# Kernel tuning notes

Hardware: AMD Instinct MI355X
Metric: run time of the kernel (lower is better)

Reference implementation:

```python
import jax, jax.numpy as jnp
import numpy as np

DIM = 1024
EPS = 1e-5

def _layernorm(x, w, b):
    mu = jnp.mean(x, axis=-1, keepdims=True)
    var = jnp.var(x, axis=-1, keepdims=True)
    return (x - mu) * jax.lax.rsqrt(var + EPS) * w + b

def setup_inputs() -> dict:
    key = jax.random.key(0)
    ks = jax.random.split(key, 16)
    d = DIM
    s = 1.0 / np.sqrt(d)
    inp = {
        "x": jax.random.normal(ks[0], (4, 2048, d), dtype=jnp.float32),
        "ln1_w": jnp.ones((d,), jnp.float32),
        "ln1_b": jnp.zeros((d,), jnp.float32),
        "Wq": jax.random.normal(ks[1], (d, d), jnp.float32) * s,
        "bq": jnp.zeros((d,), jnp.float32),
        "Wk": jax.random.normal(ks[2], (d, d), jnp.float32) * s,
        "bk": jnp.zeros((d,), jnp.float32),
        "Wv": jax.random.normal(ks[3], (d, d), jnp.float32) * s,
        "bv": jnp.zeros((d,), jnp.float32),
        "Wo": jax.random.normal(ks[4], (d, d), jnp.float32) * s,
        "bo": jnp.zeros((d,), jnp.float32),
        "W1": jax.random.normal(ks[5], (d, 4 * d), jnp.float32) * s,
        "b1": jnp.zeros((4 * d,), jnp.float32),
        "W2": jax.random.normal(ks[6], (4 * d, d), jnp.float32) * (0.5 / np.sqrt(d)),
        "b2": jnp.zeros((d,), jnp.float32),
        "ln2_w": jnp.ones((d,), jnp.float32),
        "ln2_b": jnp.zeros((d,), jnp.float32),
    }
    return inp

def reference(x, ln1_w, ln1_b, Wq, bq, Wk, bk, Wv, bv, Wo, bo, W1, b1, W2, b2, ln2_w, ln2_b):
    d = x.shape[-1]
    scale = 1.0 / jnp.sqrt(jnp.asarray(d, x.dtype))
    h = _layernorm(x, ln1_w, ln1_b)
    q = h @ Wq + bq
    k = h @ Wk + bk
    v = h @ Wv + bv
    # [b, s, s] attention scores (single head, full matrix as in original)
    scores = jnp.einsum("bqd,bkd->bqk", q, k) * scale
    attn = jax.nn.softmax(scores, axis=-1)
    ctx = jnp.einsum("bqk,bkd->bqd", attn, v)
    x = x + (ctx @ Wo + bo)
    h2 = _layernorm(x, ln2_w, ln2_b)
    ffn = jax.nn.relu(h2 @ W1 + b1) @ W2 + b2
    return x + ffn
```

## Files before the change

kernel.cpp:

```cpp
#include <hip/hip_runtime.h>


#define EPS 1e-5f
constexpr int D   = 1024;
constexpr int DFF = 4096;
constexpr int NB  = 4;
constexpr int S   = 2048;
constexpr int M   = NB * S;

typedef __bf16 bf16x8 __attribute__((ext_vector_type(8)));
typedef float  f32x4  __attribute__((ext_vector_type(4)));

__device__ __forceinline__ ushort f2bf(float f) {
  uint u = __builtin_bit_cast(uint, f);
  return (ushort)((u + 0x7fffu + ((u >> 16) & 1u)) >> 16);
}
__device__ __forceinline__ float bf2f(ushort h) {
  return __builtin_bit_cast(float, (uint)h << 16);
}
__device__ __forceinline__ void split(float f, ushort& h, ushort& l) {
  h = f2bf(f);
  l = f2bf(f - bf2f(h));
}

#define GLOAD16(g, l)                                                     \
  __builtin_amdgcn_global_load_lds(                                       \
      (const __attribute__((address_space(1))) void*)(g),                 \
      (__attribute__((address_space(3))) void*)(l), 16, 0, 0)

#define LD8(base, off) \
  __builtin_bit_cast(bf16x8, *reinterpret_cast<const uint4*>((base) + (off)))

__global__ __launch_bounds__(256) void ln_kernel(const float* __restrict__ x,
                                                 const float* __restrict__ w,
                                                 const float* __restrict__ b,
                                                 ushort* __restrict__ oh,
                                                 ushort* __restrict__ ol) {
  const int row = blockIdx.x;
  const int t   = threadIdx.x;
  const float4 v = reinterpret_cast<const float4*>(x + (size_t)row * D)[t];
  float s  = v.x + v.y + v.z + v.w;
  float sq = v.x * v.x + v.y * v.y + v.z * v.z + v.w * v.w;
#pragma unroll
  for (int off = 32; off > 0; off >>= 1) {
    s  += __shfl_down(s, off);
    sq += __shfl_down(sq, off);
  }
  __shared__ float red[8];
  if ((t & 63) == 0) { red[t >> 6] = s; red[(t >> 6) + 4] = sq; }
  __syncthreads();
  if (t == 0) {
    float ts = red[0] + red[1] + red[2] + red[3];
    float tq = red[4] + red[5] + red[6] + red[7];
    float mu  = ts * (1.0f / D);
    float var = tq * (1.0f / D) - mu * mu;
    red[0] = mu;
    red[1] = rsqrtf(var + EPS);
  }
  __syncthreads();
  const float mu = red[0], rs = red[1];
  const float4 wv = reinterpret_cast<const float4*>(w)[t];
  const float4 bv = reinterpret_cast<const float4*>(b)[t];
  float o0 = (v.x - mu) * rs * wv.x + bv.x;
  float o1 = (v.y - mu) * rs * wv.y + bv.y;
  float o2 = (v.z - mu) * rs * wv.z + bv.z;
  float o3 = (v.w - mu) * rs * wv.w + bv.w;
  ushort4 hh, ll;
  split(o0, hh.x, ll.x); split(o1, hh.y, ll.y);
  split(o2, hh.z, ll.z); split(o3, hh.w, ll.w);
  *reinterpret_cast<ushort4*>(oh + (size_t)row * D + t * 4) = hh;
  *reinterpret_cast<ushort4*>(ol + (size_t)row * D + t * 4) = ll;
}

__global__ __launch_bounds__(256) void softmax_kernel(const float* __restrict__ sc,
                                                      ushort* __restrict__ oh,
                                                      ushort* __restrict__ ol) {
  const size_t row = blockIdx.x;
  const float* p = sc + row * (size_t)S;
  const int t = threadIdx.x;
  constexpr float scale = 0.03125f;
  float4 a = reinterpret_cast<const float4*>(p)[t];
  float4 b = reinterpret_cast<const float4*>(p)[t + 256];
  a.x *= scale; a.y *= scale; a.z *= scale; a.w *= scale;
  b.x *= scale; b.y *= scale; b.z *= scale; b.w *= scale;
  float m = fmaxf(fmaxf(fmaxf(a.x, a.y), fmaxf(a.z, a.w)),
                  fmaxf(fmaxf(b.x, b.y), fmaxf(b.z, b.w)));
#pragma unroll
  for (int off = 32; off > 0; off >>= 1) m = fmaxf(m, __shfl_xor(m, off));
  __shared__ float redm[4];
  __shared__ float reds[4];
  if ((t & 63) == 0) redm[t >> 6] = m;
  __syncthreads();
  m = fmaxf(fmaxf(redm[0], redm[1]), fmaxf(redm[2], redm[3]));
  a.x = __expf(a.x - m); a.y = __expf(a.y - m);
  a.z = __expf(a.z - m); a.w = __expf(a.w - m);
  b.x = __expf(b.x - m); b.y = __expf(b.y - m);
  b.z = __expf(b.z - m); b.w = __expf(b.w - m);
  float s = a.x + a.y + a.z + a.w + b.x + b.y + b.z + b.w;
#pragma unroll
  for (int off = 32; off > 0; off >>= 1) s += __shfl_xor(s, off);
  if ((t & 63) == 0) reds[t >> 6] = s;
  __syncthreads();
  s = reds[0] + reds[1] + reds[2] + reds[3];
  const float inv = 1.0f / s;
  ushort4 ha, la, hb, lb;
  split(a.x * inv, ha.x, la.x); split(a.y * inv, ha.y, la.y);
  split(a.z * inv, ha.z, la.z); split(a.w * inv, ha.w, la.w);
  split(b.x * inv, hb.x, lb.x); split(b.y * inv, hb.y, lb.y);
  split(b.z * inv, hb.z, lb.z); split(b.w * inv, hb.w, lb.w);
  ushort* ph = oh + row * (size_t)S;
  ushort* pl = ol + row * (size_t)S;
  *reinterpret_cast<ushort4*>(ph + t * 4)        = ha;
  *reinterpret_cast<ushort4*>(ph + 1024 + t * 4) = hb;
  *reinterpret_cast<ushort4*>(pl + t * 4)        = la;
  *reinterpret_cast<ushort4*>(pl + 1024 + t * 4) = lb;
}

__global__ __launch_bounds__(256) void transpose_conv(const float* __restrict__ in,
                                                      ushort* __restrict__ oh,
                                                      ushort* __restrict__ ol,
                                                      int R, int C,
                                                      long long sIn, long long sOut) {
  __shared__ float tile[32][33];
  const int bz = blockIdx.z;
  const float* ip = in + (size_t)bz * sIn;
  ushort* ph = oh + (size_t)bz * sOut;
  ushort* pl = ol + (size_t)bz * sOut;
  const int c0 = blockIdx.x * 32, r0 = blockIdx.y * 32;
  const int tx = threadIdx.x & 31, ty = threadIdx.x >> 5;
#pragma unroll
  for (int i = 0; i < 4; ++i)
    tile[ty + 8 * i][tx] = ip[(size_t)(r0 + ty + 8 * i) * C + c0 + tx];
  __syncthreads();
#pragma unroll
  for (int i = 0; i < 4; ++i) {
    float v = tile[tx][ty + 8 * i];
    ushort h, l;
    split(v, h, l);
    const size_t o = (size_t)(c0 + ty + 8 * i) * R + r0 + tx;
    ph[o] = h;
    pl[o] = l;
  }
}

__global__ __launch_bounds__(256) void transpose_bf(const ushort* __restrict__ ih,
                                                    const ushort* __restrict__ il,
                                                    ushort* __restrict__ oh,
                                                    ushort* __restrict__ ol,
                                                    int R, int C,
                                                    long long sIn, long long sOut) {
  __shared__ ushort th[32][34];
  __shared__ ushort tl[32][34];
  const int bz = blockIdx.z;
  const ushort* ph = ih + (size_t)bz * sIn;
  const ushort* pl = il + (size_t)bz * sIn;
  ushort* qh = oh + (size_t)bz * sOut;
  ushort* ql = ol + (size_t)bz * sOut;
  const int c0 = blockIdx.x * 32, r0 = blockIdx.y * 32;
  const int tx = threadIdx.x & 31, ty = threadIdx.x >> 5;
#pragma unroll
  for (int i = 0; i < 4; ++i) {
    const size_t src = (size_t)(r0 + ty + 8 * i) * C + c0 + tx;
    th[ty + 8 * i][tx] = ph[src];
    tl[ty + 8 * i][tx] = pl[src];
  }
  __syncthreads();
#pragma unroll
  for (int i = 0; i < 4; ++i) {
    const size_t o = (size_t)(c0 + ty + 8 * i) * R + r0 + tx;
    qh[o] = th[tx][ty + 8 * i];
    ql[o] = tl[tx][ty + 8 * i];
  }
}

template <bool HAS_BIAS, bool RELU, bool WRITE_F32, int NSEG>
__global__ __launch_bounds__(512, 2) void gemm256(
    const ushort* __restrict__ Ah, const ushort* __restrict__ Al,
    const ushort* __restrict__ Bth, const ushort* __restrict__ Btl,
    const float* __restrict__ b0, const float* __restrict__ b1,
    const float* __restrict__ b2, float* __restrict__ Cf,
    ushort* __restrict__ Ch0, ushort* __restrict__ Cl0,
    ushort* __restrict__ Ch1, ushort* __restrict__ Cl1,
    ushort* __restrict__ Ch2, ushort* __restrict__ Cl2,
    int N, int K, int ostride, long long sA, long long sB, long long sC) {
  __shared__ __align__(16) ushort sAb[2][256 * 64];
  __shared__ __align__(16) ushort sBb[2][256 * 64];

  const int bz = blockIdx.z;
  const size_t aof = (size_t)bz * sA, bof = (size_t)bz * sB, cof = (size_t)bz * sC;

  const int gx = gridDim.x;
  const int nwg = gx * gridDim.y;
  int lin = blockIdx.y * gx + blockIdx.x;
  lin = (lin & 7) * (nwg >> 3) + (lin >> 3);
  const int bm = (lin / gx) * 256;
  const int bn = (lin % gx) * 256;

  const int tid = threadIdx.x;
  const int lane = tid & 63, w = tid >> 6;
  const int wr = (w >> 2) * 128, wc = (w & 3) * 64;
  const int fr = lane & 15, fc = lane >> 4;

  const int srow  = tid >> 3;
  const int slot  = (tid & 7) ^ (srow & 7);
  const int hilo  = slot >> 2;
  const int kg    = slot & 3;
  const ushort* gA = (hilo ? Al : Ah) + aof + (size_t)(bm + srow) * K + kg * 8;
  const ushort* gB = (hilo ? Btl : Bth) + bof + (size_t)(bn + srow) * K + kg * 8;
  const size_t rstep = (size_t)64 * K;
  const int dsto = tid * 16;

  int aoff[8][2], boff[4][2];
#pragma unroll
  for (int i = 0; i < 8; ++i) {
    const int row = wr + i * 16 + fr;
#pragma unroll
    for (int h = 0; h < 2; ++h)
      aoff[i][h] = row * 128 + (((h * 4 + fc) ^ (row & 7)) * 16);
  }
#pragma unroll
  for (int j = 0; j < 4; ++j) {
    const int row = wc + j * 16 + fr;
#pragma unroll
    for (int h = 0; h < 2; ++h)
      boff[j][h] = row * 128 + (((h * 4 + fc) ^ (row & 7)) * 16);
  }

  f32x4 acc[8][4];
  const f32x4 zero = {0.f, 0.f, 0.f, 0.f};
#pragma unroll
  for (int i = 0; i < 8; ++i)
#pragma unroll
    for (int j = 0; j < 4; ++j) acc[i][j] = zero;

  const int nt = K >> 5;

  {
    char* dA = (char*)(&sAb[0][0]) + dsto;
    char* dB = (char*)(&sBb[0][0]) + dsto;
#pragma unroll
    for (int rr = 0; rr < 4; ++rr) {
      GLOAD16(gA + rr * rstep, dA + rr * 8192);
      GLOAD16(gB + rr * rstep, dB + rr * 8192);
    }
  }

#define MFMA6(ii, xh, xl, jj)                                                 \
  acc[ii][jj] = __builtin_amdgcn_mfma_f32_16x16x32_bf16(xh, bh##jj, acc[ii][jj], 0, 0, 0); \
  acc[ii][jj] = __builtin_amdgcn_mfma_f32_16x16x32_bf16(xh, bl##jj, acc[ii][jj], 0, 0, 0); \
  acc[ii][jj] = __builtin_amdgcn_mfma_f32_16x16x32_bf16(xl, bh##jj, acc[ii][jj], 0, 0, 0);

#define MFMA_PAIR(i0, i1, xh, xl, yh, yl)                                     \
  MFMA6(i0, xh, xl, 0) MFMA6(i1, yh, yl, 0)                                   \
  MFMA6(i0, xh, xl, 1) MFMA6(i1, yh, yl, 1)                                   \
  MFMA6(i0, xh, xl, 2) MFMA6(i1, yh, yl, 2)                                   \
  MFMA6(i0, xh, xl, 3) MFMA6(i1, yh, yl, 3)

  for (int t = 0; t < nt; ++t) {
    const int p = t & 1, q = p ^ 1;
    const bool pf = (t + 1 < nt);
    const int kkn = (t + 1) << 5;
    const ushort* gAn = gA + kkn;
    const ushort* gBn = gB + kkn;
    char* dAq = (char*)(&sAb[q][0]) + dsto;
    char* dBq = (char*)(&sBb[q][0]) + dsto;
    const char* lA = (const char*)(&sAb[p][0]);
    const char* lB = (const char*)(&sBb[p][0]);

    if (pf) {
      GLOAD16(gAn + 0 * rstep, dAq + 0 * 8192);
      GLOAD16(gAn + 1 * rstep, dAq + 1 * 8192);
      asm volatile("s_waitcnt vmcnt(2)" ::: "memory");
    } else {
      asm volatile("s_waitcnt vmcnt(0)" ::: "memory");
    }
    __builtin_amdgcn_s_barrier();

    bf16x8 bh0 = LD8(lB, boff[0][0]), bl0 = LD8(lB, boff[0][1]);
    bf16x8 bh1 = LD8(lB, boff[1][0]), bl1 = LD8(lB, boff[1][1]);
    bf16x8 bh2 = LD8(lB, boff[2][0]), bl2 = LD8(lB, boff[2][1]);
    bf16x8 bh3 = LD8(lB, boff[3][0]), bl3 = LD8(lB, boff[3][1]);
    bf16x8 a0h = LD8(lA, aoff[0][0]), a0l = LD8(lA, aoff[0][1]);
    bf16x8 a1h = LD8(lA, aoff[1][0]), a1l = LD8(lA, aoff[1][1]);
    __builtin_amdgcn_s_barrier();
    __builtin_amdgcn_s_setprio(1);
    MFMA_PAIR(0, 1, a0h, a0l, a1h, a1l)
    __builtin_amdgcn_s_setprio(0);
    __builtin_amdgcn_s_barrier();

    {
      bf16x8 a2h = LD8(lA, aoff[2][0]), a2l = LD8(lA, aoff[2][1]);
      bf16x8 a3h = LD8(lA, aoff[3][0]), a3l = LD8(lA, aoff[3][1]);
      if (pf) {
        GLOAD16(gAn + 2 * rstep, dAq + 2 * 8192);
        GLOAD16(gAn + 3 * rstep, dAq + 3 * 8192);
      }
      __builtin_amdgcn_s_barrier();
      __builtin_amdgcn_s_setprio(1);
      MFMA_PAIR(2, 3, a2h, a2l, a3h, a3l)
      __builtin_amdgcn_s_setprio(0);
      __builtin_amdgcn_s_barrier();
    }
    {
      bf16x8 a4h = LD8(lA, aoff[4][0]), a4l = LD8(lA, aoff[4][1]);
      bf16x8 a5h = LD8(lA, aoff[5][0]), a5l = LD8(lA, aoff[5][1]);
      if (pf) {
        GLOAD16(gBn + 0 * rstep, dBq + 0 * 8192);
        GLOAD16(gBn + 1 * rstep, dBq + 1 * 8192);
      }
      __builtin_amdgcn_s_barrier();
      __builtin_amdgcn_s_setprio(1);
      MFMA_PAIR(4, 5, a4h, a4l, a5h, a5l)
      __builtin_amdgcn_s_setprio(0);
      __builtin_amdgcn_s_barrier();
    }
    {
      bf16x8 a6h = LD8(lA, aoff[6][0]), a6l = LD8(lA, aoff[6][1]);
      bf16x8 a7h = LD8(lA, aoff[7][0]), a7l = LD8(lA, aoff[7][1]);
      if (pf) {
        GLOAD16(gBn + 2 * rstep, dBq + 2 * 8192);
        GLOAD16(gBn + 3 * rstep, dBq + 3 * 8192);
      }
      __builtin_amdgcn_s_barrier();
      __builtin_amdgcn_s_setprio(1);
      MFMA_PAIR(6, 7, a6h, a6l, a7h, a7l)
      __builtin_amdgcn_s_setprio(0);
      __builtin_amdgcn_s_barrier();
    }
  }

#pragma unroll
  for (int j = 0; j < 4; ++j) {
    const int col = bn + wc + j * 16 + fr;
    int lc = col;
    const float* bp = b0;
    ushort* ph = Ch0;
    ushort* pl = Cl0;
    if (NSEG == 3) {
      const int seg = col >> 10;
      lc = col & 1023;
      bp = (seg == 0) ? b0 : (seg == 1 ? b1 : b2);
      ph = (seg == 0) ? Ch0 : (seg == 1 ? Ch1 : Ch2);
      pl = (seg == 0) ? Cl0 : (seg == 1 ? Cl1 : Cl2);
    }
    const float bi = HAS_BIAS ? bp[lc] : 0.0f;
#pragma unroll
    for (int i = 0; i < 8; ++i) {
#pragma unroll
      for (int r = 0; r < 4; ++r) {
        const int row = bm + wr + i * 16 + fc * 4 + r;
        float o = acc[i][j][r] + bi;
        if (RELU) o = fmaxf(o, 0.0f);
        if (WRITE_F32) {
          Cf[cof + (size_t)row * N + col] = o;
        } else {
          ushort hh, ll;
          split(o, hh, ll);
          const size_t idx = (size_t)row * ostride + lc;
          ph[idx] = hh;
          pl[idx] = ll;
        }
      }
    }
  }
#undef MFMA6
#undef MFMA_PAIR
}

template <bool HAS_BIAS, bool RELU, bool HAS_RES, bool WRITE_F32, bool EMIT_BF16>
__global__ __launch_bounds__(256, 2) void gemm_bf16x3(
    const ushort* __restrict__ Ah, const ushort* __restrict__ Al,
    const ushort* __restrict__ Bth, const ushort* __restrict__ Btl,
    const float* __restrict__ bias, const float* Res,
    float* Cf, ushort* __restrict__ Ch, ushort* __restrict__ Cl,
    int N, int K, long long sA, long long sB, long long sC) {
  __shared__ __align__(16) ushort sAh[128 * 32];
  __shared__ __align__(16) ushort sAl[128 * 32];
  __shared__ __align__(16) ushort sBh[128 * 32];
  __shared__ __align__(16) ushort sBl[128 * 32];

  const int bz = blockIdx.z;
  const size_t aof = (size_t)bz * sA, bof = (size_t)bz * sB, cof = (size_t)bz * sC;

  const int gx = gridDim.x;
  const int nwg = gx * gridDim.y;
  int lin = blockIdx.y * gx + blockIdx.x;
  lin = (lin & 7) * (nwg >> 3) + (lin >> 3);
  const int bm = (lin / gx) * 128;
  const int bn = (lin % gx) * 128;

  const int tid = threadIdx.x, w = tid >> 6, lane = tid & 63;
  const int wr = (w >> 1) * 64, wc = (w & 1) * 64;

  const int c0 = w * 2, c1 = c0 + 1;
  const int r0 = c0 * 16 + (lane >> 2);
  const int r1 = r0 + 16;
  const int kc = ((lane & 3) ^ (r0 & 3)) * 8;
  const size_t gA0 = aof + (size_t)(bm + r0) * K + kc;
  const size_t gA1 = aof + (size_t)(bm + r1) * K + kc;
  const size_t gB0 = bof + (size_t)(bn + r0) * K + kc;
  const size_t gB1 = bof + (size_t)(bn + r1) * K + kc;
  ushort* dA0 = sAh + c0 * 512; ushort* dA1 = sAh + c1 * 512;
  ushort* dA2 = sAl + c0 * 512; ushort* dA3 = sAl + c1 * 512;
  ushort* dB0 = sBh + c0 * 512; ushort* dB1 = sBh + c1 * 512;
  ushort* dB2 = sBl + c0 * 512; ushort* dB3 = sBl + c1 * 512;

  const int fr = lane & 15, fc = lane >> 4;
  int aoffB[4], boffB[4];
#pragma unroll
  for (int i = 0; i < 4; ++i) {
    const int ra = wr + i * 16 + fr;
    aoffB[i] = ra * 64 + ((fc ^ (ra & 3)) * 16);
    const int rb = wc + i * 16 + fr;
    boffB[i] = rb * 64 + ((fc ^ (rb & 3)) * 16);
  }

  f32x4 acc[4][4];
  const f32x4 zero = {0.f, 0.f, 0.f, 0.f};
#pragma unroll
  for (int i = 0; i < 4; ++i)
#pragma unroll
    for (int j = 0; j < 4; ++j) acc[i][j] = zero;

  for (int kk = 0; kk < K; kk += 32) {
    GLOAD16(Ah + gA0 + kk, dA0);
    GLOAD16(Ah + gA1 + kk, dA1);
    GLOAD16(Al + gA0 + kk, dA2);
    GLOAD16(Al + gA1 + kk, dA3);
    GLOAD16(Bth + gB0 + kk, dB0);
    GLOAD16(Bth + gB1 + kk, dB1);
    GLOAD16(Btl + gB0 + kk, dB2);
    GLOAD16(Btl + gB1 + kk, dB3);
    __syncthreads();

    bf16x8 fah[4], fal[4], fbh[4], fbl[4];
#pragma unroll
    for (int i = 0; i < 4; ++i) {
      fah[i] = LD8((const char*)sAh, aoffB[i]);
      fal[i] = LD8((const char*)sAl, aoffB[i]);
      fbh[i] = LD8((const char*)sBh, boffB[i]);
      fbl[i] = LD8((const char*)sBl, boffB[i]);
    }
    __syncthreads();

#pragma unroll
    for (int i = 0; i < 4; ++i)
#pragma unroll
      for (int j = 0; j < 4; ++j) {
        acc[i][j] = __builtin_amdgcn_mfma_f32_16x16x32_bf16(fah[i], fbh[j], acc[i][j], 0, 0, 0);
        acc[i][j] = __builtin_amdgcn_mfma_f32_16x16x32_bf16(fah[i], fbl[j], acc[i][j], 0, 0, 0);
        acc[i][j] = __builtin_amdgcn_mfma_f32_16x16x32_bf16(fal[i], fbh[j], acc[i][j], 0, 0, 0);
      }
  }

#pragma unroll
  for (int j = 0; j < 4; ++j) {
    const int col = bn + wc + j * 16 + fr;
    const float bi = HAS_BIAS ? bias[col] : 0.0f;
#pragma unroll
    for (int i = 0; i < 4; ++i) {
#pragma unroll
      for (int r = 0; r < 4; ++r) {
        const int row = bm + wr + i * 16 + fc * 4 + r;
        float o = acc[i][j][r] + bi;
        if (RELU) o = fmaxf(o, 0.0f);
        const size_t idx = cof + (size_t)row * N + col;
        if (HAS_RES) o += Res[idx];
        if (WRITE_F32) Cf[idx] = o;
        if (EMIT_BF16) {
          ushort h, l;
          split(o, h, l);
          Ch[idx] = h;
          Cl[idx] = l;
        }
      }
    }
  }
}

extern "C" void kernel_launch(void* const* d_in, const int* in_sizes, int n_in,
                              void* d_out, int out_size, void* d_ws, size_t ws_size,
                              hipStream_t stream) {
  const float* x     = (const float*)d_in[0];
  const float* ln1_w = (const float*)d_in[1];
  const float* ln1_b = (const float*)d_in[2];
  const float* Wq    = (const float*)d_in[3];
  const float* bq    = (const float*)d_in[4];
  const float* Wk    = (const float*)d_in[5];
  const float* bk    = (const float*)d_in[6];
  const float* Wv    = (const float*)d_in[7];
  const float* bv    = (const float*)d_in[8];
  const float* Wo    = (const float*)d_in[9];
  const float* bo    = (const float*)d_in[10];
  const float* W1    = (const float*)d_in[11];
  const float* b1    = (const float*)d_in[12];
  const float* W2    = (const float*)d_in[13];
  const float* b2    = (const float*)d_in[14];
  const float* ln2_w = (const float*)d_in[15];
  const float* ln2_b = (const float*)d_in[16];
  float* out = (float*)d_out;
  char* W = (char*)d_ws;

  auto U = [&](size_t mb) { return (ushort*)(W + (mb << 20)); };
  auto F = [&](size_t mb) { return (float*)(W + (mb << 20)); };
  ushort *h1h = U(0),   *h1l = U(16);
  ushort *wqkvh = U(32), *wqkvl = U(38);
  ushort *qh  = U(64),  *ql  = U(80);
  ushort *kh  = U(96),  *kl  = U(112);
  ushort *vh  = U(128), *vl  = U(144);
  ushort *vth = U(160), *vtl = U(176);
  float  *scf = F(0);
  ushort *ath = U(64),  *atl = U(96);
  ushort *cxh = U(128), *cxl = U(144);
  ushort *woh = U(0),   *wol = U(2);
  ushort *h2h = U(4),   *h2l = U(20);
  ushort *w1h = U(36),  *w1l = U(44);
  ushort *w2h = U(0),   *w2l = U(8);
  ushort *t1h = U(64),  *t1l = U(128);

  const long long SD = (long long)S * D, SS = (long long)S * S;
  dim3 tb(256);

  transpose_conv<<<dim3(32, 32, 1), tb, 0, stream>>>(Wq, wqkvh, wqkvl, D, D, 0, 0);
  transpose_conv<<<dim3(32, 32, 1), tb, 0, stream>>>(Wk, wqkvh + (size_t)D * D,
                                                     wqkvl + (size_t)D * D, D, D, 0, 0);
  transpose_conv<<<dim3(32, 32, 1), tb, 0, stream>>>(Wv, wqkvh + 2 * (size_t)D * D,
                                                     wqkvl + 2 * (size_t)D * D, D, D, 0, 0);

  ln_kernel<<<M, tb, 0, stream>>>(x, ln1_w, ln1_b, h1h, h1l);

  gemm256<true, false, false, 3><<<dim3(12, 32, 1), 512, 0, stream>>>(
      h1h, h1l, wqkvh, wqkvl, bq, bk, bv, nullptr,
      qh, ql, kh, kl, vh, vl, 3072, D, D, 0, 0, 0);

  transpose_bf<<<dim3(32, 64, NB), tb, 0, stream>>>(vh, vl, vth, vtl, S, D, SD, SD);

  gemm256<false, false, true, 1><<<dim3(8, 8, NB), 512, 0, stream>>>(
      qh, ql, kh, kl, nullptr, nullptr, nullptr, scf,
      nullptr, nullptr, nullptr, nullptr, nullptr, nullptr,
      S, D, S, SD, SD, SS);

  softmax_kernel<<<M, tb, 0, stream>>>(scf, ath, atl);

  gemm_bf16x3<false, false, false, false, true><<<dim3(8, 16, NB), tb, 0, stream>>>(
      ath, atl, vth, vtl, nullptr, nullptr, nullptr, cxh, cxl, D, S, SS, SD, SD);

  transpose_conv<<<dim3(32, 32, 1), tb, 0, stream>>>(Wo, woh, wol, D, D, 0, 0);
  gemm_bf16x3<true, false, true, true, false><<<dim3(8, 64, 1), tb, 0, stream>>>(
      cxh, cxl, woh, wol, bo, x, out, nullptr, nullptr, D, D, 0, 0, 0);

  ln_kernel<<<M, tb, 0, stream>>>(out, ln2_w, ln2_b, h2h, h2l);

  transpose_conv<<<dim3(128, 32, 1), tb, 0, stream>>>(W1, w1h, w1l, D, DFF, 0, 0);

  gemm256<true, true, false, 1><<<dim3(16, 32, 1), 512, 0, stream>>>(
      h2h, h2l, w1h, w1l, b1, nullptr, nullptr, nullptr,
      t1h, t1l, nullptr, nullptr, nullptr, nullptr, DFF, D, DFF, 0, 0, 0);

  transpose_conv<<<dim3(32, 128, 1), tb, 0, stream>>>(W2, w2h, w2l, DFF, D, 0, 0);

  gemm_bf16x3<true, false, true, true, false><<<dim3(8, 64, 1), tb, 0, stream>>>(
      t1h, t1l, w2h, w2l, b2, out, out, nullptr, nullptr, D, DFF, 0, 0, 0);
}
```

Measured before the change: 1.075 ms.

## Double-buffer 128-tile GEMM, simplify gemm256 prefetch, split fused QKV projection

The 128x128 GEMM becomes gemm128p. It holds hi/lo tiles interleaved in a double-buffered, XOR-swizzled LDS layout, prefetches the next K-tile with async global-to-LDS loads, and removes the two __syncthreads per iteration. gemm256 now issues all eight prefetch loads at the top of each iteration and drops several barriers. The fused 3-segment QKV GEMM is replaced by three separate gemm128p launches. The aim is to overlap global loads with MFMA work and cut barrier overhead, but it costs more kernel launches, lower tile reuse for QKV, and possible LDS-reuse hazards from the removed barriers.

Measured after the change: 1.062 ms. No clear change (-1.1%).

```diff
diff --git a/kernel.cpp b/kernel.cpp
--- a/kernel.cpp
+++ b/kernel.cpp
@@ -30,6 +30,17 @@
 
 #define LD8(base, off) \
   __builtin_bit_cast(bf16x8, *reinterpret_cast<const uint4*>((base) + (off)))
+
+#define MFMA6(ii, xh, xl, jj)                                                 \
+  acc[ii][jj] = __builtin_amdgcn_mfma_f32_16x16x32_bf16(xh, bh##jj, acc[ii][jj], 0, 0, 0); \
+  acc[ii][jj] = __builtin_amdgcn_mfma_f32_16x16x32_bf16(xh, bl##jj, acc[ii][jj], 0, 0, 0); \
+  acc[ii][jj] = __builtin_amdgcn_mfma_f32_16x16x32_bf16(xl, bh##jj, acc[ii][jj], 0, 0, 0);
+
+#define MFMA_PAIR(i0, i1, xh, xl, yh, yl)                                     \
+  MFMA6(i0, xh, xl, 0) MFMA6(i1, yh, yl, 0)                                   \
+  MFMA6(i0, xh, xl, 1) MFMA6(i1, yh, yl, 1)                                   \
+  MFMA6(i0, xh, xl, 2) MFMA6(i1, yh, yl, 2)                                   \
+  MFMA6(i0, xh, xl, 3) MFMA6(i1, yh, yl, 3)
 
 __global__ __launch_bounds__(256) void ln_kernel(const float* __restrict__ x,
                                                  const float* __restrict__ w,
@@ -173,15 +184,12 @@
   }
 }
 
-template <bool HAS_BIAS, bool RELU, bool WRITE_F32, int NSEG>
+template <bool HAS_BIAS, bool RELU, bool WRITE_F32>
 __global__ __launch_bounds__(512, 2) void gemm256(
     const ushort* __restrict__ Ah, const ushort* __restrict__ Al,
     const ushort* __restrict__ Bth, const ushort* __restrict__ Btl,
-    const float* __restrict__ b0, const float* __restrict__ b1,
-    const float* __restrict__ b2, float* __restrict__ Cf,
-    ushort* __restrict__ Ch0, ushort* __restrict__ Cl0,
-    ushort* __restrict__ Ch1, ushort* __restrict__ Cl1,
-    ushort* __restrict__ Ch2, ushort* __restrict__ Cl2,
+    const float* __restrict__ bias, float* __restrict__ Cf,
+    ushort* __restrict__ Ch, ushort* __restrict__ Cl,
     int N, int K, int ostride, long long sA, long long sB, long long sC) {
   __shared__ __align__(16) ushort sAb[2][256 * 64];
   __shared__ __align__(16) ushort sBb[2][256 * 64];
@@ -245,32 +253,21 @@
     }
   }
 
-#define MFMA6(ii, xh, xl, jj)                                                 \
-  acc[ii][jj] = __builtin_amdgcn_mfma_f32_16x16x32_bf16(xh, bh##jj, acc[ii][jj], 0, 0, 0); \
-  acc[ii][jj] = __builtin_amdgcn_mfma_f32_16x16x32_bf16(xh, bl##jj, acc[ii][jj], 0, 0, 0); \
-  acc[ii][jj] = __builtin_amdgcn_mfma_f32_16x16x32_bf16(xl, bh##jj, acc[ii][jj], 0, 0, 0);
-
-#define MFMA_PAIR(i0, i1, xh, xl, yh, yl)                                     \
-  MFMA6(i0, xh, xl, 0) MFMA6(i1, yh, yl, 0)                                   \
-  MFMA6(i0, xh, xl, 1) MFMA6(i1, yh, yl, 1)                                   \
-  MFMA6(i0, xh, xl, 2) MFMA6(i1, yh, yl, 2)                                   \
-  MFMA6(i0, xh, xl, 3) MFMA6(i1, yh, yl, 3)
-
   for (int t = 0; t < nt; ++t) {
     const int p = t & 1, q = p ^ 1;
-    const bool pf = (t + 1 < nt);
-    const int kkn = (t + 1) << 5;
-    const ushort* gAn = gA + kkn;
-    const ushort* gBn = gB + kkn;
-    char* dAq = (char*)(&sAb[q][0]) + dsto;
-    char* dBq = (char*)(&sBb[q][0]) + dsto;
     const char* lA = (const char*)(&sAb[p][0]);
     const char* lB = (const char*)(&sBb[p][0]);
-
-    if (pf) {
-      GLOAD16(gAn + 0 * rstep, dAq + 0 * 8192);
-      GLOAD16(gAn + 1 * rstep, dAq + 1 * 8192);
-      asm volatile("s_waitcnt vmcnt(2)" ::: "memory");
+    if (t + 1 < nt) {
+      const ushort* gAn = gA + ((t + 1) << 5);
+      const ushort* gBn = gB + ((t + 1) << 5);
+      char* dAq = (char*)(&sAb[q][0]) + dsto;
+      char* dBq = (char*)(&sBb[q][0]) + dsto;
+#pragma unroll
+      for (int rr = 0; rr < 4; ++rr) {
+        GLOAD16(gAn + rr * rstep, dAq + rr * 8192);
+        GLOAD16(gBn + rr * rstep, dBq + rr * 8192);
+      }
+      asm volatile("s_waitcnt vmcnt(8)" ::: "memory");
     } else {
       asm volatile("s_waitcnt vmcnt(0)" ::: "memory");
     }
@@ -282,20 +279,13 @@
     bf16x8 bh3 = LD8(lB, boff[3][0]), bl3 = LD8(lB, boff[3][1]);
     bf16x8 a0h = LD8(lA, aoff[0][0]), a0l = LD8(lA, aoff[0][1]);
     bf16x8 a1h = LD8(lA, aoff[1][0]), a1l = LD8(lA, aoff[1][1]);
-    __builtin_amdgcn_s_barrier();
     __builtin_amdgcn_s_setprio(1);
     MFMA_PAIR(0, 1, a0h, a0l, a1h, a1l)
     __builtin_amdgcn_s_setprio(0);
     __builtin_amdgcn_s_barrier();
-
     {
       bf16x8 a2h = LD8(lA, aoff[2][0]), a2l = LD8(lA, aoff[2][1]);
       bf16x8 a3h = LD8(lA, aoff[3][0]), a3l = LD8(lA, aoff[3][1]);
-      if (pf) {
-        GLOAD16(gAn + 2 * rstep, dAq + 2 * 8192);
-        GLOAD16(gAn + 3 * rstep, dAq + 3 * 8192);
-      }
-      __builtin_amdgcn_s_barrier();
       __builtin_amdgcn_s_setprio(1);
       MFMA_PAIR(2, 3, a2h, a2l, a3h, a3l)
       __builtin_amdgcn_s_setprio(0);
@@ -304,11 +294,6 @@
     {
       bf16x8 a4h = LD8(lA, aoff[4][0]), a4l = LD8(lA, aoff[4][1]);
       bf16x8 a5h = LD8(lA, aoff[5][0]), a5l = LD8(lA, aoff[5][1]);
-      if (pf) {
-        GLOAD16(gBn + 0 * rstep, dBq + 0 * 8192);
-        GLOAD16(gBn + 1 * rstep, dBq + 1 * 8192);
-      }
-      __builtin_amdgcn_s_barrier();
       __builtin_amdgcn_s_setprio(1);
       MFMA_PAIR(4, 5, a4h, a4l, a5h, a5l)
       __builtin_amdgcn_s_setprio(0);
@@ -317,11 +302,6 @@
     {
       bf16x8 a6h = LD8(lA, aoff[6][0]), a6l = LD8(lA, aoff[6][1]);
       bf16x8 a7h = LD8(lA, aoff[7][0]), a7l = LD8(lA, aoff[7][1]);
-      if (pf) {
-        GLOAD16(gBn + 2 * rstep, dBq + 2 * 8192);
-        GLOAD16(gBn + 3 * rstep, dBq + 3 * 8192);
-      }
-      __builtin_amdgcn_s_barrier();
       __builtin_amdgcn_s_setprio(1);
       MFMA_PAIR(6, 7, a6h, a6l, a7h, a7l)
       __builtin_amdgcn_s_setprio(0);
@@ -332,18 +312,7 @@
 #pragma unroll
   for (int j = 0; j < 4; ++j) {
     const int col = bn + wc + j * 16 + fr;
-    int lc = col;
-    const float* bp = b0;
-    ushort* ph = Ch0;
-    ushort* pl = Cl0;
-    if (NSEG == 3) {
-      const int seg = col >> 10;
-      lc = col & 1023;
-      bp = (seg == 0) ? b0 : (seg == 1 ? b1 : b2);
-      ph = (seg == 0) ? Ch0 : (seg == 1 ? Ch1 : Ch2);
-      pl = (seg == 0) ? Cl0 : (seg == 1 ? Cl1 : Cl2);
-    }
-    const float bi = HAS_BIAS ? bp[lc] : 0.0f;
+    const float bi = HAS_BIAS ? bias[col] : 0.0f;
 #pragma unroll
     for (int i = 0; i < 8; ++i) {
 #pragma unroll
@@ -356,28 +325,24 @@
         } else {
           ushort hh, ll;
           split(o, hh, ll);
-          const size_t idx = (size_t)row * ostride + lc;
-          ph[idx] = hh;
-          pl[idx] = ll;
+          const size_t idx = (size_t)row * ostride + col;
+          Ch[idx] = hh;
+          Cl[idx] = ll;
         }
       }
     }
   }
-#undef MFMA6
-#undef MFMA_PAIR
 }
 
 template <bool HAS_BIAS, bool RELU, bool HAS_RES, bool WRITE_F32, bool EMIT_BF16>
-__global__ __launch_bounds__(256, 2) void gemm_bf16x3(
+__global__ __launch_bounds__(256, 2) void gemm128p(
     const ushort* __restrict__ Ah, const ushort* __restrict__ Al,
     const ushort* __restrict__ Bth, const ushort* __restrict__ Btl,
     const float* __restrict__ bias, const float* Res,
     float* Cf, ushort* __restrict__ Ch, ushort* __restrict__ Cl,
     int N, int K, long long sA, long long sB, long long sC) {
-  __shared__ __align__(16) ushort sAh[128 * 32];
-  __shared__ __align__(16) ushort sAl[128 * 32];
-  __shared__ __align__(16) ushort sBh[128 * 32];
-  __shared__ __align__(16) ushort sBl[128 * 32];
+  __shared__ __align__(16) ushort sAb[2][128 * 64];
+  __shared__ __align__(16) ushort sBb[2][128 * 64];
 
   const int bz = blockIdx.z;
   const size_t aof = (size_t)bz * sA, bof = (size_t)bz * sB, cof = (size_t)bz * sC;
@@ -389,30 +354,30 @@
   const int bm = (lin / gx) * 128;
   const int bn = (lin % gx) * 128;
 
-  const int tid = threadIdx.x, w = tid >> 6, lane = tid & 63;
+  const int tid = threadIdx.x;
+  const int lane = tid & 63, w = tid >> 6;
   const int wr = (w >> 1) * 64, wc = (w & 1) * 64;
-
-  const int c0 = w * 2, c1 = c0 + 1;
-  const int r0 = c0 * 16 + (lane >> 2);
-  const int r1 = r0 + 16;
-  const int kc = ((lane & 3) ^ (r0 & 3)) * 8;
-  const size_t gA0 = aof + (size_t)(bm + r0) * K + kc;
-  const size_t gA1 = aof + (size_t)(bm + r1) * K + kc;
-  const size_t gB0 = bof + (size_t)(bn + r0) * K + kc;
-  const size_t gB1 = bof + (size_t)(bn + r1) * K + kc;
-  ushort* dA0 = sAh + c0 * 512; ushort* dA1 = sAh + c1 * 512;
-  ushort* dA2 = sAl + c0 * 512; ushort* dA3 = sAl + c1 * 512;
-  ushort* dB0 = sBh + c0 * 512; ushort* dB1 = sBh + c1 * 512;
-  ushort* dB2 = sBl + c0 * 512; ushort* dB3 = sBl + c1 * 512;
-
   const int fr = lane & 15, fc = lane >> 4;
-  int aoffB[4], boffB[4];
+
+  const int srow  = tid >> 3;
+  const int slot  = (tid & 7) ^ (srow & 7);
+  const int hilo  = slot >> 2;
+  const int kg    = slot & 3;
+  const ushort* gA = (hilo ? Al : Ah) + aof + (size_t)(bm + srow) * K + kg * 8;
+  const ushort* gB = (hilo ? Btl : Bth) + bof + (size_t)(bn + srow) * K + kg * 8;
+  const size_t rstep = (size_t)32 * K;
+  const int dsto = tid * 16;
+
+  int aoff[4][2], boff[4][2];
 #pragma unroll
   for (int i = 0; i < 4; ++i) {
     const int ra = wr + i * 16 + fr;
-    aoffB[i] = ra * 64 + ((fc ^ (ra & 3)) * 16);
     const int rb = wc + i * 16 + fr;
-    boffB[i] = rb * 64 + ((fc ^ (rb & 3)) * 16);
+#pragma unroll
+    for (int h = 0; h < 2; ++h) {
+      aoff[i][h] = ra * 128 + (((h * 4 + fc) ^ (ra & 7)) * 16);
+      boff[i][h] = rb * 128 + (((h * 4 + fc) ^ (rb & 7)) * 16);
+    }
   }
 
   f32x4 acc[4][4];
@@ -422,35 +387,56 @@
 #pragma unroll
     for (int j = 0; j < 4; ++j) acc[i][j] = zero;
 
-  for (int kk = 0; kk < K; kk += 32) {
-    GLOAD16(Ah + gA0 + kk, dA0);
-    GLOAD16(Ah + gA1 + kk, dA1);
-    GLOAD16(Al + gA0 + kk, dA2);
-    GLOAD16(Al + gA1 + kk, dA3);
-    GLOAD16(Bth + gB0 + kk, dB0);
-    GLOAD16(Bth + gB1 + kk, dB1);
-    GLOAD16(Btl + gB0 + kk, dB2);
-    GLOAD16(Btl + gB1 + kk, dB3);
-    __syncthreads();
-
-    bf16x8 fah[4], fal[4], fbh[4], fbl[4];
-#pragma unroll
-    for (int i = 0; i < 4; ++i) {
-      fah[i] = LD8((const char*)sAh, aoffB[i]);
-      fal[i] = LD8((const char*)sAl, aoffB[i]);
-      fbh[i] = LD8((const char*)sBh, boffB[i]);
-      fbl[i] = LD8((const char*)sBl, boffB[i]);
-    }
-    __syncthreads();
-
-#pragma unroll
-    for (int i = 0; i < 4; ++i)
-#pragma unroll
-      for (int j = 0; j < 4; ++j) {
-        acc[i][j] = __builtin_amdgcn_mfma_f32_16x16x32_bf16(fah[i], fbh[j], acc[i][j], 0, 0, 0);
-        acc[i][j] = __builtin_amdgcn_mfma_f32_16x16x32_bf16(fah[i], fbl[j], acc[i][j], 0, 0, 0);
-        acc[i][j] = __builtin_amdgcn_mfma_f32_16x16x32_bf16(fal[i], fbh[j], acc[i][j], 0, 0, 0);
+  const int nt = K >> 5;
+
+  {
+    char* dA = (char*)(&sAb[0][0]) + dsto;
+    char* dB = (char*)(&sBb[0][0]) + dsto;
+#pragma unroll
+    for (int rr = 0; rr < 4; ++rr) {
+      GLOAD16(gA + rr * rstep, dA + rr * 4096);
+      GLOAD16(gB + rr * rstep, dB + rr * 4096);
+    }
+  }
+
+  for (int t = 0; t < nt; ++t) {
+    const int p = t & 1, q = p ^ 1;
+    const char* lA = (const char*)(&sAb[p][0]);
+    const char* lB = (const char*)(&sBb[p][0]);
+    if (t + 1 < nt) {
+      const ushort* gAn = gA + ((t + 1) << 5);
+      const ushort* gBn = gB + ((t + 1) << 5);
+      char* dAq = (char*)(&sAb[q][0]) + dsto;
+      char* dBq = (char*)(&sBb[q][0]) + dsto;
+#pragma unroll
+      for (int rr = 0; rr < 4; ++rr) {
+        GLOAD16(gAn + rr * rstep, dAq + rr * 4096);
+        GLOAD16(gBn + rr * rstep, dBq + rr * 4096);
       }
+      asm volatile("s_waitcnt vmcnt(8)" ::: "memory");
+    } else {
+      asm volatile("s_waitcnt vmcnt(0)" ::: "memory");
+    }
+    __builtin_amdgcn_s_barrier();
+
+    bf16x8 bh0 = LD8(lB, boff[0][0]), bl0 = LD8(lB, boff[0][1]);
+    bf16x8 bh1 = LD8(lB, boff[1][0]), bl1 = LD8(lB, boff[1][1]);
+    bf16x8 bh2 = LD8(lB, boff[2][0]), bl2 = LD8(lB, boff[2][1]);
+    bf16x8 bh3 = LD8(lB, boff[3][0]), bl3 = LD8(lB, boff[3][1]);
+    bf16x8 a0h = LD8(lA, aoff[0][0]), a0l = LD8(lA, aoff[0][1]);
+    bf16x8 a1h = LD8(lA, aoff[1][0]), a1l = LD8(lA, aoff[1][1]);
+    __builtin_amdgcn_s_setprio(1);
+    MFMA_PAIR(0, 1, a0h, a0l, a1h, a1l)
+    __builtin_amdgcn_s_setprio(0);
+    __builtin_amdgcn_s_barrier();
+    {
+      bf16x8 a2h = LD8(lA, aoff[2][0]), a2l = LD8(lA, aoff[2][1]);
+      bf16x8 a3h = LD8(lA, aoff[3][0]), a3l = LD8(lA, aoff[3][1]);
+      __builtin_amdgcn_s_setprio(1);
+      MFMA_PAIR(2, 3, a2h, a2l, a3h, a3l)
+      __builtin_amdgcn_s_setprio(0);
+      __builtin_amdgcn_s_barrier();
+    }
   }
 
 #pragma unroll
@@ -504,7 +490,9 @@
   auto U = [&](size_t mb) { return (ushort*)(W + (mb << 20)); };
   auto F = [&](size_t mb) { return (float*)(W + (mb << 20)); };
   ushort *h1h = U(0),   *h1l = U(16);
-  ushort *wqkvh = U(32), *wqkvl = U(38);
+  ushort *wqh = U(32),  *wql = U(34);
+  ushort *wkh = U(36),  *wkl = U(38);
+  ushort *wvh = U(40),  *wvl = U(42);
   ushort *qh  = U(64),  *ql  = U(80);
   ushort *kh  = U(96),  *kl  = U(112);
   ushort *vh  = U(128), *vl  = U(144);
@@ -521,44 +509,43 @@
   const long long SD = (long long)S * D, SS = (long long)S * S;
   dim3 tb(256);
 
-  transpose_conv<<<dim3(32, 32, 1), tb, 0, stream>>>(Wq, wqkvh, wqkvl, D, D, 0, 0);
-  transpose_conv<<<dim3(32, 32, 1), tb, 0, stream>>>(Wk, wqkvh + (size_t)D * D,
-                                                     wqkvl + (size_t)D * D, D, D, 0, 0);
-  transpose_conv<<<dim3(32, 32, 1), tb, 0, stream>>>(Wv, wqkvh + 2 * (size_t)D * D,
-                                                     wqkvl + 2 * (size_t)D * D, D, D, 0, 0);
+  transpose_conv<<<dim3(32, 32, 1), tb, 0, stream>>>(Wq, wqh, wql, D, D, 0, 0);
+  transpose_conv<<<dim3(32, 32, 1), tb, 0, stream>>>(Wk, wkh, wkl, D, D, 0, 0);
+  transpose_conv<<<dim3(32, 32, 1), tb, 0, stream>>>(Wv, wvh, wvl, D, D, 0, 0);
 
   ln_kernel<<<M, tb, 0, stream>>>(x, ln1_w, ln1_b, h1h, h1l);
 
-  gemm256<true, false, false, 3><<<dim3(12, 32, 1), 512, 0, stream>>>(
-      h1h, h1l, wqkvh, wqkvl, bq, bk, bv, nullptr,
-      qh, ql, kh, kl, vh, vl, 3072, D, D, 0, 0, 0);
+  dim3 g1024(8, 64, 1);
+  gemm128p<true, false, false, false, true><<<g1024, tb, 0, stream>>>(
+      h1h, h1l, wqh, wql, bq, nullptr, nullptr, qh, ql, D, D, 0, 0, 0);
+  gemm128p<true, false, false, false, true><<<g1024, tb, 0, stream>>>(
+      h1h, h1l, wkh, wkl, bk, nullptr, nullptr, kh, kl, D, D, 0, 0, 0);
+  gemm128p<true, false, false, false, true><<<g1024, tb, 0, stream>>>(
+      h1h, h1l, wvh, wvl, bv, nullptr, nullptr, vh, vl, D, D, 0, 0, 0);
 
   transpose_bf<<<dim3(32, 64, NB), tb, 0, stream>>>(vh, vl, vth, vtl, S, D, SD, SD);
 
-  gemm256<false, false, true, 1><<<dim3(8, 8, NB), 512, 0, stream>>>(
-      qh, ql, kh, kl, nullptr, nullptr, nullptr, scf,
-      nullptr, nullptr, nullptr, nullptr, nullptr, nullptr,
-      S, D, S, SD, SD, SS);
+  gemm256<false, false, true><<<dim3(8, 8, NB), 512, 0, stream>>>(
+      qh, ql, kh, kl, nullptr, scf, nullptr, nullptr, S, D, S, SD, SD, SS);
 
   softmax_kernel<<<M, tb, 0, stream>>>(scf, ath, atl);
 
-  gemm_bf16x3<false, false, false, false, true><<<dim3(8, 16, NB), tb, 0, stream>>>(
+  gemm128p<false, false, false, false, true><<<dim3(8, 16, NB), tb, 0, stream>>>(
       ath, atl, vth, vtl, nullptr, nullptr, nullptr, cxh, cxl, D, S, SS, SD, SD);
 
   transpose_conv<<<dim3(32, 32, 1), tb, 0, stream>>>(Wo, woh, wol, D, D, 0, 0);
-  gemm_bf16x3<true, false, true, true, false><<<dim3(8, 64, 1), tb, 0, stream>>>(
+  gemm128p<true, false, true, true, false><<<g1024, tb, 0, stream>>>(
       cxh, cxl, woh, wol, bo, x, out, nullptr, nullptr, D, D, 0, 0, 0);
 
   ln_kernel<<<M, tb, 0, stream>>>(out, ln2_w, ln2_b, h2h, h2l);
 
   transpose_conv<<<dim3(128, 32, 1), tb, 0, stream>>>(W1, w1h, w1l, D, DFF, 0, 0);
 
-  gemm256<true, true, false, 1><<<dim3(16, 32, 1), 512, 0, stream>>>(
-      h2h, h2l, w1h, w1l, b1, nullptr, nullptr, nullptr,
-      t1h, t1l, nullptr, nullptr, nullptr, nullptr, DFF, D, DFF, 0, 0, 0);
+  gemm256<true, true, false><<<dim3(16, 32, 1), 512, 0, stream>>>(
+      h2h, h2l, w1h, w1l, b1, nullptr, t1h, t1l, DFF, D, DFF, 0, 0, 0);
 
   transpose_conv<<<dim3(32, 128, 1), tb, 0, stream>>>(W2, w2h, w2l, DFF, D, 0, 0);
 
-  gemm_bf16x3<true, false, true, true, false><<<dim3(8, 64, 1), tb, 0, stream>>>(
+  gemm128p<true, false, true, true, false><<<g1024, tb, 0, stream>>>(
       t1h, t1l, w2h, w2l, b2, out, out, nullptr, nullptr, D, DFF, 0, 0, 0);
 }
```
